# Optimization experiments

Hardware: AMD Instinct MI355X
Metric: run time of the kernel (lower is better)

## Reference

```python
import jax, jax.numpy as jnp
import numpy as np

N, E = 100000, 1600000
F_IN, F_HID, F_OUT = 64, 64, 16


def setup_inputs() -> dict:
    key = jax.random.key(0)
    ks = jax.random.split(key, 10)
    def g(k, shape):
        return jax.random.normal(k, shape, dtype=jnp.float32) * 0.05
    return {
        "x": jax.random.normal(ks[0], (N, F_IN), dtype=jnp.float32),
        "adj": jax.random.randint(ks[1], (2, E), 0, N, dtype=jnp.int32),
        # ChebConv K=2 params: per-order weights [in, out] + shared bias
        "W1_0": g(ks[2], (F_IN, F_HID)), "W1_1": g(ks[3], (F_IN, F_HID)),
        "b1": jnp.zeros((F_HID,), jnp.float32),
        "Wx_0": g(ks[4], (F_HID, F_HID)), "Wx_1": g(ks[5], (F_HID, F_HID)),
        "bx": jnp.zeros((F_HID,), jnp.float32),
        "W2_0": g(ks[6], (F_HID, F_OUT)), "W2_1": g(ks[7], (F_HID, F_OUT)),
        "b2": jnp.zeros((F_OUT,), jnp.float32),
    }


def _cheb(x, row, col, w, W0, W1, b):
    # K=2 Chebyshev conv: Tx0 = x, Tx1 = L_hat @ x (sparse propagate)
    n = x.shape[0]
    tx1 = jax.ops.segment_sum(w[:, None] * x[col], row, num_segments=n)
    return x @ W0 + tx1 @ W1 + b


def reference(x, adj, W1_0, W1_1, b1, Wx_0, Wx_1, bx, W2_0, W2_1, b2):
    row, col = adj[0], adj[1]
    n = x.shape[0]
    # sym-normalized Laplacian scaled by 2/lambda_max (=1): diagonal cancels,
    # off-diagonal weight = -deg^{-1/2}[row] * deg^{-1/2}[col]
    deg = jax.ops.segment_sum(jnp.ones(adj.shape[1], x.dtype), row, num_segments=n)
    dis = jnp.where(deg > 0, jax.lax.rsqrt(jnp.maximum(deg, 1e-12)), 0.0)
    w = -dis[row] * dis[col]
    h = jax.nn.relu(_cheb(x, row, col, w, W1_0, W1_1, b1))
    # dropout is identity in eval mode
    h = jax.nn.relu(_cheb(h, row, col, w, Wx_0, Wx_1, bx))
    return _cheb(h, row, col, w, W2_0, W2_1, b2)
```

## Files before the change

kernel.cpp:

```cpp
#include <hip/hip_runtime.h>
#include <hip/hip_bf16.h>


#define EPB 4096

typedef __attribute__((ext_vector_type(8))) short bf16x8;
typedef __attribute__((ext_vector_type(4))) float f32x4;

__device__ __forceinline__ float bf2f(unsigned short u) {
    unsigned int x = ((unsigned int)u) << 16;
    return __uint_as_float(x);
}
__device__ __forceinline__ unsigned short f2bf(float f) {
    unsigned int b = __float_as_uint(f);
    unsigned int r = (b + 0x7FFF + ((b >> 16) & 1)) >> 16;
    return (unsigned short)r;
}
__device__ __forceinline__ void acc8(float* a, bf16x8 v) {
#pragma unroll
    for (int i = 0; i < 8; ++i) a[i] += bf2f((unsigned short)(short)v[i]);
}

template <int NC>
__device__ __forceinline__ void pack_pair(const float* __restrict__ W0,
                                          const float* __restrict__ W1,
                                          unsigned short* __restrict__ out, int idx) {
    constexpr int NT = NC / 16;
    int i = idx & 7;
    int m = (idx >> 3) & 15;
    int g = (idx >> 7) & 3;
    int f = idx >> 9;
    int nt = f % NT;
    int kt = f / NT;
    const float* W = (kt < 2) ? W0 : W1;
    int k = (kt & 1) * 32 + g * 8 + i;
    out[idx] = f2bf(W[k * NC + nt * 16 + m]);
}

__global__ __launch_bounds__(256) void wconv_all(const float* __restrict__ W1_0,
                                                 const float* __restrict__ W1_1,
                                                 const float* __restrict__ Wx_0,
                                                 const float* __restrict__ Wx_1,
                                                 const float* __restrict__ W2_0,
                                                 const float* __restrict__ W2_1,
                                                 unsigned short* __restrict__ wp1,
                                                 unsigned short* __restrict__ wpx,
                                                 unsigned short* __restrict__ wp2,
                                                 int* __restrict__ bcnt, int nbk) {
    int idx = blockIdx.x * 256 + threadIdx.x;
    if (idx < nbk) bcnt[idx] = 0;
    if (idx < 8192) pack_pair<64>(W1_0, W1_1, wp1, idx);
    else if (idx < 16384) pack_pair<64>(Wx_0, Wx_1, wpx, idx - 8192);
    else if (idx < 18432) pack_pair<16>(W2_0, W2_1, wp2, idx - 16384);
}

__global__ __launch_bounds__(256) void bucket_count(const int* __restrict__ row,
                                                    int* __restrict__ bcnt,
                                                    int e, int nbk) {
    __shared__ int bh[512];
    int tid = threadIdx.x;
    for (int j = tid; j < nbk; j += 256) bh[j] = 0;
    __syncthreads();
    int base = blockIdx.x * EPB;
#pragma unroll
    for (int k = 0; k < EPB / 256; ++k) {
        int i = base + k * 256 + tid;
        if (i < e) atomicAdd(&bh[row[i] >> 8], 1);
    }
    __syncthreads();
    for (int j = tid; j < nbk; j += 256) {
        int c = bh[j];
        if (c) atomicAdd(&bcnt[j], c);
    }
}

__global__ __launch_bounds__(256) void bucket_scan(const int* __restrict__ bcnt,
                                                   int* __restrict__ bbase,
                                                   int* __restrict__ bcursor,
                                                   int* __restrict__ off,
                                                   int nbk, int n, int e) {
    __shared__ int sa[512], sb[512];
    int tid = threadIdx.x;
    for (int j = tid; j < 512; j += 256) sa[j] = (j < nbk) ? bcnt[j] : 0;
    __syncthreads();
    int* in = sa;
    int* out = sb;
    for (int d = 1; d < 512; d <<= 1) {
        for (int j = tid; j < 512; j += 256)
            out[j] = in[j] + ((j >= d) ? in[j - d] : 0);
        __syncthreads();
        int* t = in; in = out; out = t;
    }
    for (int j = tid; j < nbk; j += 256) {
        int incl = in[j];
        int excl = incl - bcnt[j];
        bbase[j] = excl;
        bcursor[j] = excl;
        if (j == nbk - 1) bbase[nbk] = incl;
    }
    if (tid == 0) off[n] = e;
}

__global__ __launch_bounds__(256) void bucket_scatter(const int* __restrict__ row,
                                                      const int* __restrict__ col,
                                                      int* __restrict__ bcursor,
                                                      int* __restrict__ packed,
                                                      int e, int nbk) {
    __shared__ int bh[512];
    __shared__ int bbase[512];
    __shared__ int bcur[512];
    int tid = threadIdx.x;
    for (int j = tid; j < nbk; j += 256) { bh[j] = 0; bcur[j] = 0; }
    __syncthreads();
    int base = blockIdx.x * EPB;
#pragma unroll
    for (int k = 0; k < EPB / 256; ++k) {
        int i = base + k * 256 + tid;
        if (i < e) atomicAdd(&bh[row[i] >> 8], 1);
    }
    __syncthreads();
    for (int j = tid; j < nbk; j += 256) {
        int c = bh[j];
        bbase[j] = c ? atomicAdd(&bcursor[j], c) : 0;
    }
    __syncthreads();
#pragma unroll
    for (int k = 0; k < EPB / 256; ++k) {
        int i = base + k * 256 + tid;
        if (i < e) {
            int r = row[i];
            int b = r >> 8;
            int slot = bbase[b] + atomicAdd(&bcur[b], 1);
            packed[slot] = ((r & 255) << 17) | col[i];
        }
    }
}

__global__ __launch_bounds__(256) void bucket_build(const int* __restrict__ packed,
                                                    const int* __restrict__ bbase,
                                                    const float* __restrict__ x,
                                                    int* __restrict__ off,
                                                    float* __restrict__ dis,
                                                    int* __restrict__ csr,
                                                    unsigned short* __restrict__ y,
                                                    unsigned short* __restrict__ xb,
                                                    int n) {
    __shared__ int rcnt[256];
    __shared__ int sa[256], sb[256];
    __shared__ float disv[256];
    int tid = threadIdx.x;
    int b = blockIdx.x;
    int ebase = bbase[b], eend = bbase[b + 1];
    rcnt[tid] = 0;
    __syncthreads();
    for (int e = ebase + tid; e < eend; e += 256)
        atomicAdd(&rcnt[packed[e] >> 17], 1);
    __syncthreads();
    sa[tid] = rcnt[tid];
    __syncthreads();
    int* in = sa;
    int* out = sb;
    for (int d = 1; d < 256; d <<= 1) {
        out[tid] = in[tid] + ((tid >= d) ? in[tid - d] : 0);
        __syncthreads();
        int* t = in; in = out; out = t;
    }
    int grow = b * 256 + tid;
    int c = rcnt[tid];
    int excl = in[tid] - c;
    float dv = (c > 0) ? rsqrtf((float)c) : 0.0f;
    disv[tid] = dv;
    if (grow < n) {
        off[grow] = ebase + excl;
        dis[grow] = dv;
    }
    out[tid] = excl;
    __syncthreads();
    for (int e = ebase + tid; e < eend; e += 256) {
        int p = packed[e];
        int lr = p >> 17;
        int pos = atomicAdd(&out[lr], 1);
        csr[ebase + pos] = p & 0x1FFFF;
    }
    for (int idx = tid; idx < 4096; idx += 256) {
        int rr = idx >> 4, q = idx & 15;
        int R = b * 256 + rr;
        if (R < n) {
            float d = disv[rr];
            float4 v = ((const float4*)x)[(size_t)R * 16 + q];
            ushort4 o = {f2bf(v.x * d), f2bf(v.y * d), f2bf(v.z * d), f2bf(v.w * d)};
            ((ushort4*)y)[(size_t)R * 16 + q] = o;
            ushort4 xo = {f2bf(v.x), f2bf(v.y), f2bf(v.z), f2bf(v.w)};
            ((ushort4*)xb)[(size_t)R * 16 + q] = xo;
        }
    }
}


template <int NC, bool RELU, bool WRITE_HY>
__global__ __launch_bounds__(256) void agg_dense(const unsigned short* __restrict__ y,
                                                 const unsigned short* __restrict__ A0,
                                                 const int* __restrict__ csr,
                                                 const int* __restrict__ off,
                                                 const float* __restrict__ dis,
                                                 const unsigned short* __restrict__ Wp,
                                                 const float* __restrict__ bias,
                                                 unsigned short* __restrict__ hout,
                                                 unsigned short* __restrict__ yout,
                                                 float* __restrict__ fout,
                                                 int n) {
    constexpr int NT2 = (NC == 64) ? 2 : 1;
    __shared__ unsigned short txl[32 * 64];
    int tid = threadIdx.x;

    int row_l = tid >> 3;
    int fo = (tid & 7) * 8;
    int r = blockIdx.x * 32 + row_l;
    float a8[8];
#pragma unroll
    for (int i = 0; i < 8; ++i) a8[i] = 0.f;
    float d = 0.f;
    if (r < n) {
        int s0 = off[r], e1 = off[r + 1];
        const unsigned short* Yb = y + fo;
        int t = s0;
        for (; t + 8 <= e1; t += 8) {
            int c0 = csr[t], c1 = csr[t + 1], c2 = csr[t + 2], c3 = csr[t + 3];
            int c4 = csr[t + 4], c5 = csr[t + 5], c6 = csr[t + 6], c7 = csr[t + 7];
            bf16x8 v0 = *(const bf16x8*)(Yb + (size_t)c0 * 64);
            bf16x8 v1 = *(const bf16x8*)(Yb + (size_t)c1 * 64);
            bf16x8 v2 = *(const bf16x8*)(Yb + (size_t)c2 * 64);
            bf16x8 v3 = *(const bf16x8*)(Yb + (size_t)c3 * 64);
            bf16x8 v4 = *(const bf16x8*)(Yb + (size_t)c4 * 64);
            bf16x8 v5 = *(const bf16x8*)(Yb + (size_t)c5 * 64);
            bf16x8 v6 = *(const bf16x8*)(Yb + (size_t)c6 * 64);
            bf16x8 v7 = *(const bf16x8*)(Yb + (size_t)c7 * 64);
            acc8(a8, v0); acc8(a8, v1); acc8(a8, v2); acc8(a8, v3);
            acc8(a8, v4); acc8(a8, v5); acc8(a8, v6); acc8(a8, v7);
        }
        for (; t < e1; ++t) {
            int c = csr[t];
            bf16x8 v = *(const bf16x8*)(Yb + (size_t)c * 64);
            acc8(a8, v);
        }
        d = -dis[r];
    }
    bf16x8 ov;
#pragma unroll
    for (int i = 0; i < 8; ++i) ov[i] = (short)f2bf(a8[i] * d);
    int swz = (row_l & 7) << 4;
    *(bf16x8*)((char*)txl + row_l * 128 + ((fo * 2) ^ swz)) = ov;
    __syncthreads();

    int lane = tid & 63;
    int m = lane & 15;
    int g = lane >> 4;
    int w = tid >> 6;
    int t16 = (NC == 64) ? (w >> 1) : w;
    int ch = (NC == 64) ? (w & 1) : 0;
    if (NC == 16 && w >= 2) return;
    const bf16x8* WP = (const bf16x8*)Wp;
    bf16x8 bf[NT2][4];
#pragma unroll
    for (int kt = 0; kt < 4; ++kt)
#pragma unroll
        for (int nt = 0; nt < NT2; ++nt)
            bf[nt][kt] = WP[((kt * (NC / 16) + ch * NT2 + nt) * 4 + g) * 16 + m];
    int r0 = blockIdx.x * 32 + t16 * 16;
    int ra = r0 + m;
    if (ra > n - 1) ra = n - 1;
    const unsigned short* q0 = A0 + (size_t)ra * 64 + g * 8;
    bf16x8 a0 = *(const bf16x8*)q0;
    bf16x8 a1 = *(const bf16x8*)(q0 + 32);
    int rl2 = t16 * 16 + m;
    int sw2 = (m & 7) << 4;
    bf16x8 a2 = *(bf16x8*)((char*)txl + rl2 * 128 + ((g * 16) ^ sw2));
    bf16x8 a3 = *(bf16x8*)((char*)txl + rl2 * 128 + ((64 + g * 16) ^ sw2));
    f32x4 acc[NT2];
#pragma unroll
    for (int nt = 0; nt < NT2; ++nt) {
        float b = bias[(ch * NT2 + nt) * 16 + m];
        acc[nt][0] = b; acc[nt][1] = b; acc[nt][2] = b; acc[nt][3] = b;
    }
#pragma unroll
    for (int nt = 0; nt < NT2; ++nt) {
        acc[nt] = __builtin_amdgcn_mfma_f32_16x16x32_bf16(a0, bf[nt][0], acc[nt], 0, 0, 0);
        acc[nt] = __builtin_amdgcn_mfma_f32_16x16x32_bf16(a1, bf[nt][1], acc[nt], 0, 0, 0);
        acc[nt] = __builtin_amdgcn_mfma_f32_16x16x32_bf16(a2, bf[nt][2], acc[nt], 0, 0, 0);
        acc[nt] = __builtin_amdgcn_mfma_f32_16x16x32_bf16(a3, bf[nt][3], acc[nt], 0, 0, 0);
    }
#pragma unroll
    for (int reg = 0; reg < 4; ++reg) {
        int rr = r0 + 4 * g + reg;
        if (rr >= n) continue;
        if (WRITE_HY) {
            float dv = dis[rr];
#pragma unroll
            for (int nt = 0; nt < NT2; ++nt) {
                int cc = (ch * NT2 + nt) * 16 + m;
                float v = acc[nt][reg];
                if (RELU) v = fmaxf(v, 0.f);
                hout[(size_t)rr * NC + cc] = f2bf(v);
                yout[(size_t)rr * NC + cc] = f2bf(v * dv);
            }
        } else {
#pragma unroll
            for (int nt = 0; nt < NT2; ++nt)
                fout[(size_t)rr * NC + (ch * NT2 + nt) * 16 + m] = acc[nt][reg];
        }
    }
}


extern "C" void kernel_launch(void* const* d_in, const int* in_sizes, int n_in,
                              void* d_out, int out_size, void* d_ws, size_t ws_size,
                              hipStream_t stream) {
    const float* x    = (const float*)d_in[0];
    const int*   adj  = (const int*)d_in[1];
    const float* W1_0 = (const float*)d_in[2];
    const float* W1_1 = (const float*)d_in[3];
    const float* b1   = (const float*)d_in[4];
    const float* Wx_0 = (const float*)d_in[5];
    const float* Wx_1 = (const float*)d_in[6];
    const float* bx   = (const float*)d_in[7];
    const float* W2_0 = (const float*)d_in[8];
    const float* W2_1 = (const float*)d_in[9];
    const float* b2   = (const float*)d_in[10];
    float* out = (float*)d_out;

    int N = in_sizes[0] / 64;
    int E = in_sizes[1] / 2;
    const int* row = adj;
    const int* col = adj + E;
    int NBK = (N + 255) / 256;

    char* p = (char*)d_ws;
    auto alloc = [&](size_t bytes) {
        char* q = p;
        p += (bytes + 255) & ~(size_t)255;
        return q;
    };
    int*   bcnt  = (int*)alloc((size_t)(NBK) * 4);
    int*   bbase = (int*)alloc((size_t)(NBK + 1) * 4);
    int*   bcur  = (int*)alloc((size_t)(NBK) * 4);
    int*   off   = (int*)alloc((size_t)(N + 1) * 4);
    float* dis   = (float*)alloc((size_t)N * 4);
    int*   csr   = (int*)alloc((size_t)E * 4);
    int*   packed = (int*)alloc((size_t)E * 4);
    unsigned short* wp1 = (unsigned short*)alloc(8192 * 2);
    unsigned short* wpx = (unsigned short*)alloc(8192 * 2);
    unsigned short* wp2 = (unsigned short*)alloc(2048 * 2);
    unsigned short* y  = (unsigned short*)alloc((size_t)N * 64 * 2);
    unsigned short* y2 = (unsigned short*)alloc((size_t)N * 64 * 2);
    unsigned short* xb = (unsigned short*)alloc((size_t)N * 64 * 2);
    unsigned short* h  = (unsigned short*)alloc((size_t)N * 64 * 2);
    unsigned short* h2 = (unsigned short*)alloc((size_t)N * 64 * 2);
    (void)ws_size;

    int EB = (E + EPB - 1) / EPB;
    wconv_all<<<72, 256, 0, stream>>>(W1_0, W1_1, Wx_0, Wx_1, W2_0, W2_1,
                                      wp1, wpx, wp2, bcnt, NBK);
    bucket_count<<<EB, 256, 0, stream>>>(row, bcnt, E, NBK);
    bucket_scan<<<1, 256, 0, stream>>>(bcnt, bbase, bcur, off, NBK, N, E);
    bucket_scatter<<<EB, 256, 0, stream>>>(row, col, bcur, packed, E, NBK);
    bucket_build<<<NBK, 256, 0, stream>>>(packed, bbase, x, off, dis, csr, y, xb, N);

    int nb32 = (N + 31) / 32;
    agg_dense<64, true, true><<<nb32, 256, 0, stream>>>(y, xb, csr, off, dis, wp1, b1, h, y2, nullptr, N);
    agg_dense<64, true, true><<<nb32, 256, 0, stream>>>(y2, h, csr, off, dis, wpx, bx, h2, y, nullptr, N);
    agg_dense<16, false, false><<<nb32, 256, 0, stream>>>(y, h2, csr, off, dis, wp2, b2, nullptr, nullptr, out, N);
}
```

Before: 204.4 us.

## Use 16 threads per row with 8-byte gathers and masked unrolled neighbor loop

The aggregation kernel now assigns 16 threads per destination row, each gathering 4 bf16 features (8 bytes) instead of 8 threads gathering 16 bytes, and processes 16 rows per block. The neighbor loop always issues 8 clamped gathers per iteration with masked accumulation, removing the scalar tail loop so more loads stay in flight. The MFMA epilogue is reshaped so each wave handles one 16-column tile of a 16-row block. This raises memory-level parallelism per row at the cost of narrower loads, redundant clamped loads for short rows, and twice as many blocks.

```diff
diff --git a/kernel.cpp b/kernel.cpp
--- a/kernel.cpp
+++ b/kernel.cpp
@@ -16,9 +16,14 @@
     unsigned int r = (b + 0x7FFF + ((b >> 16) & 1)) >> 16;
     return (unsigned short)r;
 }
-__device__ __forceinline__ void acc8(float* a, bf16x8 v) {
-#pragma unroll
-    for (int i = 0; i < 8; ++i) a[i] += bf2f((unsigned short)(short)v[i]);
+__device__ __forceinline__ void acc4(float* a, ushort4 v) {
+    a[0] += bf2f(v.x); a[1] += bf2f(v.y); a[2] += bf2f(v.z); a[3] += bf2f(v.w);
+}
+__device__ __forceinline__ void acc4m(float* a, ushort4 v, bool m) {
+    a[0] += m ? bf2f(v.x) : 0.0f;
+    a[1] += m ? bf2f(v.y) : 0.0f;
+    a[2] += m ? bf2f(v.z) : 0.0f;
+    a[3] += m ? bf2f(v.w) : 0.0f;
 }
 
 template <int NC>
@@ -209,104 +214,90 @@
                                                  unsigned short* __restrict__ yout,
                                                  float* __restrict__ fout,
                                                  int n) {
-    constexpr int NT2 = (NC == 64) ? 2 : 1;
-    __shared__ unsigned short txl[32 * 64];
-    int tid = threadIdx.x;
-
-    int row_l = tid >> 3;
-    int fo = (tid & 7) * 8;
-    int r = blockIdx.x * 32 + row_l;
-    float a8[8];
-#pragma unroll
-    for (int i = 0; i < 8; ++i) a8[i] = 0.f;
+    __shared__ unsigned short txl[16 * 64];
+    int tid = threadIdx.x;
+
+    int row_l = tid >> 4;
+    int q = tid & 15;
+    int r = blockIdx.x * 16 + row_l;
+    float a4[4] = {0.f, 0.f, 0.f, 0.f};
     float d = 0.f;
     if (r < n) {
         int s0 = off[r], e1 = off[r + 1];
-        const unsigned short* Yb = y + fo;
-        int t = s0;
-        for (; t + 8 <= e1; t += 8) {
-            int c0 = csr[t], c1 = csr[t + 1], c2 = csr[t + 2], c3 = csr[t + 3];
-            int c4 = csr[t + 4], c5 = csr[t + 5], c6 = csr[t + 6], c7 = csr[t + 7];
-            bf16x8 v0 = *(const bf16x8*)(Yb + (size_t)c0 * 64);
-            bf16x8 v1 = *(const bf16x8*)(Yb + (size_t)c1 * 64);
-            bf16x8 v2 = *(const bf16x8*)(Yb + (size_t)c2 * 64);
-            bf16x8 v3 = *(const bf16x8*)(Yb + (size_t)c3 * 64);
-            bf16x8 v4 = *(const bf16x8*)(Yb + (size_t)c4 * 64);
-            bf16x8 v5 = *(const bf16x8*)(Yb + (size_t)c5 * 64);
-            bf16x8 v6 = *(const bf16x8*)(Yb + (size_t)c6 * 64);
-            bf16x8 v7 = *(const bf16x8*)(Yb + (size_t)c7 * 64);
-            acc8(a8, v0); acc8(a8, v1); acc8(a8, v2); acc8(a8, v3);
-            acc8(a8, v4); acc8(a8, v5); acc8(a8, v6); acc8(a8, v7);
-        }
-        for (; t < e1; ++t) {
-            int c = csr[t];
-            bf16x8 v = *(const bf16x8*)(Yb + (size_t)c * 64);
-            acc8(a8, v);
+        int e1m = e1 - 1;
+        const unsigned short* Yq = y + q * 4;
+        for (int t = s0; t < e1; t += 8) {
+            int i1 = (t + 1 < e1) ? t + 1 : e1m;
+            int i2 = (t + 2 < e1) ? t + 2 : e1m;
+            int i3 = (t + 3 < e1) ? t + 3 : e1m;
+            int i4 = (t + 4 < e1) ? t + 4 : e1m;
+            int i5 = (t + 5 < e1) ? t + 5 : e1m;
+            int i6 = (t + 6 < e1) ? t + 6 : e1m;
+            int i7 = (t + 7 < e1) ? t + 7 : e1m;
+            int c0 = csr[t],  c1 = csr[i1], c2 = csr[i2], c3 = csr[i3];
+            int c4 = csr[i4], c5 = csr[i5], c6 = csr[i6], c7 = csr[i7];
+            ushort4 v0 = *(const ushort4*)(Yq + (size_t)c0 * 64);
+            ushort4 v1 = *(const ushort4*)(Yq + (size_t)c1 * 64);
+            ushort4 v2 = *(const ushort4*)(Yq + (size_t)c2 * 64);
+            ushort4 v3 = *(const ushort4*)(Yq + (size_t)c3 * 64);
+            ushort4 v4 = *(const ushort4*)(Yq + (size_t)c4 * 64);
+            ushort4 v5 = *(const ushort4*)(Yq + (size_t)c5 * 64);
+            ushort4 v6 = *(const ushort4*)(Yq + (size_t)c6 * 64);
+            ushort4 v7 = *(const ushort4*)(Yq + (size_t)c7 * 64);
+            bool m1 = t + 1 < e1, m2 = t + 2 < e1, m3 = t + 3 < e1;
+            bool m4 = t + 4 < e1, m5 = t + 5 < e1, m6 = t + 6 < e1, m7 = t + 7 < e1;
+            acc4(a4, v0);
+            acc4m(a4, v1, m1); acc4m(a4, v2, m2); acc4m(a4, v3, m3);
+            acc4m(a4, v4, m4); acc4m(a4, v5, m5); acc4m(a4, v6, m6); acc4m(a4, v7, m7);
         }
         d = -dis[r];
     }
-    bf16x8 ov;
-#pragma unroll
-    for (int i = 0; i < 8; ++i) ov[i] = (short)f2bf(a8[i] * d);
-    int swz = (row_l & 7) << 4;
-    *(bf16x8*)((char*)txl + row_l * 128 + ((fo * 2) ^ swz)) = ov;
+    ushort4 ov = {f2bf(a4[0] * d), f2bf(a4[1] * d), f2bf(a4[2] * d), f2bf(a4[3] * d)};
+    *(ushort4*)((char*)txl + row_l * 128 + ((q * 8) ^ ((row_l & 7) << 4))) = ov;
     __syncthreads();
 
     int lane = tid & 63;
     int m = lane & 15;
     int g = lane >> 4;
     int w = tid >> 6;
-    int t16 = (NC == 64) ? (w >> 1) : w;
-    int ch = (NC == 64) ? (w & 1) : 0;
-    if (NC == 16 && w >= 2) return;
+    if (NC == 16 && w > 0) return;
+    int we = (NC == 64) ? w : 0;
     const bf16x8* WP = (const bf16x8*)Wp;
-    bf16x8 bf[NT2][4];
+    bf16x8 bfr[4];
 #pragma unroll
     for (int kt = 0; kt < 4; ++kt)
-#pragma unroll
-        for (int nt = 0; nt < NT2; ++nt)
-            bf[nt][kt] = WP[((kt * (NC / 16) + ch * NT2 + nt) * 4 + g) * 16 + m];
-    int r0 = blockIdx.x * 32 + t16 * 16;
+        bfr[kt] = WP[((kt * (NC / 16) + we) * 4 + g) * 16 + m];
+    int r0 = blockIdx.x * 16;
     int ra = r0 + m;
     if (ra > n - 1) ra = n - 1;
     const unsigned short* q0 = A0 + (size_t)ra * 64 + g * 8;
     bf16x8 a0 = *(const bf16x8*)q0;
     bf16x8 a1 = *(const bf16x8*)(q0 + 32);
-    int rl2 = t16 * 16 + m;
     int sw2 = (m & 7) << 4;
-    bf16x8 a2 = *(bf16x8*)((char*)txl + rl2 * 128 + ((g * 16) ^ sw2));
-    bf16x8 a3 = *(bf16x8*)((char*)txl + rl2 * 128 + ((64 + g * 16) ^ sw2));
-    f32x4 acc[NT2];
-#pragma unroll
-    for (int nt = 0; nt < NT2; ++nt) {
-        float b = bias[(ch * NT2 + nt) * 16 + m];
-        acc[nt][0] = b; acc[nt][1] = b; acc[nt][2] = b; acc[nt][3] = b;
-    }
-#pragma unroll
-    for (int nt = 0; nt < NT2; ++nt) {
-        acc[nt] = __builtin_amdgcn_mfma_f32_16x16x32_bf16(a0, bf[nt][0], acc[nt], 0, 0, 0);
-        acc[nt] = __builtin_amdgcn_mfma_f32_16x16x32_bf16(a1, bf[nt][1], acc[nt], 0, 0, 0);
-        acc[nt] = __builtin_amdgcn_mfma_f32_16x16x32_bf16(a2, bf[nt][2], acc[nt], 0, 0, 0);
-        acc[nt] = __builtin_amdgcn_mfma_f32_16x16x32_bf16(a3, bf[nt][3], acc[nt], 0, 0, 0);
-    }
+    bf16x8 a2 = *(bf16x8*)((char*)txl + m * 128 + ((g * 16) ^ sw2));
+    bf16x8 a3 = *(bf16x8*)((char*)txl + m * 128 + ((64 + g * 16) ^ sw2));
+    f32x4 acc;
+    {
+        float b = bias[we * 16 + m];
+        acc[0] = b; acc[1] = b; acc[2] = b; acc[3] = b;
+    }
+    acc = __builtin_amdgcn_mfma_f32_16x16x32_bf16(a0, bfr[0], acc, 0, 0, 0);
+    acc = __builtin_amdgcn_mfma_f32_16x16x32_bf16(a1, bfr[1], acc, 0, 0, 0);
+    acc = __builtin_amdgcn_mfma_f32_16x16x32_bf16(a2, bfr[2], acc, 0, 0, 0);
+    acc = __builtin_amdgcn_mfma_f32_16x16x32_bf16(a3, bfr[3], acc, 0, 0, 0);
 #pragma unroll
     for (int reg = 0; reg < 4; ++reg) {
         int rr = r0 + 4 * g + reg;
         if (rr >= n) continue;
+        int cc = we * 16 + m;
         if (WRITE_HY) {
             float dv = dis[rr];
-#pragma unroll
-            for (int nt = 0; nt < NT2; ++nt) {
-                int cc = (ch * NT2 + nt) * 16 + m;
-                float v = acc[nt][reg];
-                if (RELU) v = fmaxf(v, 0.f);
-                hout[(size_t)rr * NC + cc] = f2bf(v);
-                yout[(size_t)rr * NC + cc] = f2bf(v * dv);
-            }
+            float v = acc[reg];
+            if (RELU) v = fmaxf(v, 0.f);
+            hout[(size_t)rr * NC + cc] = f2bf(v);
+            yout[(size_t)rr * NC + cc] = f2bf(v * dv);
         } else {
-#pragma unroll
-            for (int nt = 0; nt < NT2; ++nt)
-                fout[(size_t)rr * NC + (ch * NT2 + nt) * 16 + m] = acc[nt][reg];
+            fout[(size_t)rr * NC + cc] = acc[reg];
         }
     }
 }
@@ -365,8 +356,8 @@
     bucket_scatter<<<EB, 256, 0, stream>>>(row, col, bcur, packed, E, NBK);
     bucket_build<<<NBK, 256, 0, stream>>>(packed, bbase, x, off, dis, csr, y, xb, N);
 
-    int nb32 = (N + 31) / 32;
-    agg_dense<64, true, true><<<nb32, 256, 0, stream>>>(y, xb, csr, off, dis, wp1, b1, h, y2, nullptr, N);
-    agg_dense<64, true, true><<<nb32, 256, 0, stream>>>(y2, h, csr, off, dis, wpx, bx, h2, y, nullptr, N);
-    agg_dense<16, false, false><<<nb32, 256, 0, stream>>>(y, h2, csr, off, dis, wp2, b2, nullptr, nullptr, out, N);
-}
+    int nb16 = (N + 15) / 16;
+    agg_dense<64, true, true><<<nb16, 256, 0, stream>>>(y, xb, csr, off, dis, wp1, b1, h, y2, nullptr, N);
+    agg_dense<64, true, true><<<nb16, 256, 0, stream>>>(y2, h, csr, off, dis, wpx, bx, h2, y, nullptr, N);
+    agg_dense<16, false, false><<<nb16, 256, 0, stream>>>(y, h2, csr, off, dis, wp2, b2, nullptr, nullptr, out, N);
+}
```

New measurement: 193.8 us. 1.05x faster.
